# Optimization experiments

Measured on AMD Instinct MI355X. Metric: run time of the kernel, lower is better.

Reference implementation:

```python
import jax, jax.numpy as jnp
import numpy as np

EPS = 1e-12  # matches torch F.normalize default eps

def _l2_normalize(x):
    # torch.nn.functional.normalize: x / max(||x||_2, eps)
    n = jnp.sqrt(jnp.sum(x * x, axis=-1, keepdims=True))
    return x / jnp.maximum(n, EPS)

def setup_inputs() -> dict:
    key = jax.random.key(0)
    kq, kk, kv = jax.random.split(key, 3)
    B, N, M, C = 8, 4096, 4096, 256
    return {
        "query": jax.random.normal(kq, (B, N, C), dtype=jnp.float32),
        "key": jax.random.normal(kk, (B, M, C), dtype=jnp.float32),
        "value": jax.random.normal(kv, (B, M, C), dtype=jnp.float32),
    }

def reference(query, key, value):
    B, N, C = query.shape
    q = _l2_normalize(query)          # (B, N, C)
    k = _l2_normalize(key)            # (B, M, C)
    kv = jnp.einsum('bmc,bmd->bcd', k, value)   # (B, C, C)
    context = jnp.einsum('bnc,bcd->bnd', q, kv) # (B, N, C)
    return context / N
```

## Files before the change

### kernel.cpp

```cpp
#include <hip/hip_runtime.h>

typedef __attribute__((ext_vector_type(4))) float v4f;
typedef __attribute__((ext_vector_type(8))) short short8;
typedef unsigned short u16;
typedef __attribute__((ext_vector_type(4))) unsigned short u16x4;
typedef __attribute__((ext_vector_type(8))) unsigned short u16x8;

#define CDIM 256
#define NB 8
#define NN 4096
#define MM 4096

static __device__ __forceinline__ u16 f2bf(float f) {
  unsigned u = __float_as_uint(f);
  u = (u + 0x7fffu + ((u >> 16) & 1u)) >> 16;
  return (u16)u;
}
static __device__ __forceinline__ float bf2f(u16 h) {
  return __uint_as_float(((unsigned)h) << 16);
}

__global__ __launch_bounds__(256) void knorm_kernel(const float* __restrict__ key,
                                                    float* __restrict__ sk) {
  int t = threadIdx.x;
  int lane = t & 63;
  int r = blockIdx.x * 4 + (t >> 6);
  const v4f x = *(const v4f*)(key + (size_t)r * CDIM + lane * 4);
  float ss = x[0]*x[0] + x[1]*x[1] + x[2]*x[2] + x[3]*x[3];
  #pragma unroll
  for (int m = 1; m < 64; m <<= 1) ss += __shfl_xor(ss, m);
  if (lane == 0) sk[r] = 1.0f / fmaxf(sqrtf(ss), 1e-12f);
}

__global__ __launch_bounds__(512, 2) void kv_kernel(const float* __restrict__ key,
                                                    const float* __restrict__ value,
                                                    const float* __restrict__ sk,
                                                    u16* __restrict__ partial, int KC) {
  __shared__ __align__(16) u16 knT[256 * 64];
  __shared__ __align__(16) u16 vT[256 * 64];
  int t = threadIdx.x;
  int b = blockIdx.y, s = blockIdx.x;
  int w = t >> 6, lane = t & 63, lo = lane & 15, hi = lane >> 4;
  int cstage = t & 255, wq = t >> 8;

  v4f acc[2][16];
  #pragma unroll
  for (int i = 0; i < 2; i++)
    #pragma unroll
    for (int d = 0; d < 16; d++) acc[i][d] = (v4f){0.f, 0.f, 0.f, 0.f};

  int nsc = KC >> 6;
  for (int sc = 0; sc < nsc; ++sc) {
    int mbase = s * KC + sc * 64;
    #pragma unroll
    for (int it = 0; it < 8; ++it) {
      int ml0 = it * 8 + wq * 4;
      int gr = b * MM + mbase + ml0;
      size_t grow = (size_t)gr * CDIM + cstage;
      float k0 = key[grow], k1 = key[grow + CDIM], k2 = key[grow + 2 * CDIM], k3 = key[grow + 3 * CDIM];
      float s0 = sk[gr], s1 = sk[gr + 1], s2 = sk[gr + 2], s3 = sk[gr + 3];
      u16x4 kn = { f2bf(k0 * s0), f2bf(k1 * s1), f2bf(k2 * s2), f2bf(k3 * s3) };
      int idx = (cstage * 64 + ml0) ^ ((cstage & 7) << 3);
      *(u16x4*)&knT[idx] = kn;
      float v0 = value[grow], v1 = value[grow + CDIM], v2 = value[grow + 2 * CDIM], v3 = value[grow + 3 * CDIM];
      u16x4 vn = { f2bf(v0), f2bf(v1), f2bf(v2), f2bf(v3) };
      *(u16x4*)&vT[idx] = vn;
    }
    __syncthreads();
    #pragma unroll
    for (int kk = 0; kk < 64; kk += 32) {
      int acol = kk + hi * 8;
      int r0 = w * 32 + lo, r1 = w * 32 + 16 + lo;
      short8 a0 = *(const short8*)&knT[(r0 * 64 + acol) ^ ((r0 & 7) << 3)];
      short8 a1 = *(const short8*)&knT[(r1 * 64 + acol) ^ ((r1 & 7) << 3)];
      #pragma unroll
      for (int dt = 0; dt < 16; ++dt) {
        int drow = dt * 16 + lo;
        short8 bb = *(const short8*)&vT[(drow * 64 + acol) ^ ((drow & 7) << 3)];
        acc[0][dt] = __builtin_amdgcn_mfma_f32_16x16x32_bf16(bb, a0, acc[0][dt], 0, 0, 0);
        acc[1][dt] = __builtin_amdgcn_mfma_f32_16x16x32_bf16(bb, a1, acc[1][dt], 0, 0, 0);
      }
    }
    __syncthreads();
  }
  size_t base = ((size_t)(s * NB + b)) << 16;
  #pragma unroll
  for (int i = 0; i < 2; i++) {
    int cc = w * 32 + i * 16 + lo;
    #pragma unroll
    for (int dt = 0; dt < 16; ++dt) {
      int dd = dt * 16 + hi * 4;
      #pragma unroll
      for (int r = 0; r < 4; r++)
        partial[base + (size_t)(dd + r) * 256 + cc] = f2bf(acc[i][dt][r]);
    }
  }
}

__global__ __launch_bounds__(256) void red_kernel(const u16* __restrict__ partial,
                                                  u16* __restrict__ kvT, int splits) {
  int j = blockIdx.x * 256 + threadIdx.x;
  int b = j >> 13;
  int e0 = (j & 8191) * 8;
  size_t off = ((size_t)b << 16) + e0;
  const float inv = 1.0f / 4096.0f;
  float sum[8] = {0.f, 0.f, 0.f, 0.f, 0.f, 0.f, 0.f, 0.f};
  for (int s = 0; s < splits; ++s) {
    u16x8 p = *(const u16x8*)&partial[(((size_t)s * NB) << 16) + off];
    #pragma unroll
    for (int x = 0; x < 8; ++x) sum[x] += bf2f(p[x]);
  }
  u16x8 o;
  #pragma unroll
  for (int x = 0; x < 8; ++x) o[x] = f2bf(sum[x] * inv);
  *(u16x8*)&kvT[off] = o;
}

__global__ __launch_bounds__(512) void ctx_kernel(const float* __restrict__ query,
                                                  const u16* __restrict__ kvT,
                                                  float* __restrict__ out) {
  __shared__ __align__(16) u16 qn[2][16 * 256];
  int t = threadIdx.x;
  int b = blockIdx.y;
  int tile0 = blockIdx.x * 4;
  int w = t >> 6, lane = t & 63, lo = lane & 15, hi = lane >> 4;
  int row = t >> 5, l32 = t & 31;
  const float* qbase = query + (size_t)b * NN * CDIM + (size_t)row * CDIM + l32 * 8;

  const float* qr0 = qbase + (size_t)(tile0 * 16) * CDIM;
  v4f x0 = *(const v4f*)qr0;
  v4f x1 = *(const v4f*)(qr0 + 4);

  const u16* kvb = kvT + ((size_t)b << 16);
  short8 Bf[2][8];
  #pragma unroll
  for (int i = 0; i < 2; i++) {
    int dr = (2 * w + i) * 16 + lo;
    #pragma unroll
    for (int kc = 0; kc < 8; kc++)
      Bf[i][kc] = *(const short8*)&kvb[(size_t)dr * 256 + kc * 32 + 8 * hi];
  }

  {
    float ss = x0[0]*x0[0] + x0[1]*x0[1] + x0[2]*x0[2] + x0[3]*x0[3]
             + x1[0]*x1[0] + x1[1]*x1[1] + x1[2]*x1[2] + x1[3]*x1[3];
    #pragma unroll
    for (int m = 1; m < 32; m <<= 1) ss += __shfl_xor(ss, m);
    float sc = 1.0f / fmaxf(sqrtf(ss), 1e-12f);
    u16x8 qb;
    qb[0] = f2bf(x0[0] * sc); qb[1] = f2bf(x0[1] * sc);
    qb[2] = f2bf(x0[2] * sc); qb[3] = f2bf(x0[3] * sc);
    qb[4] = f2bf(x1[0] * sc); qb[5] = f2bf(x1[1] * sc);
    qb[6] = f2bf(x1[2] * sc); qb[7] = f2bf(x1[3] * sc);
    *(u16x8*)&qn[0][(row * 256 + l32 * 8) ^ ((row & 7) << 3)] = qb;
  }

  int cur = 0;
  #pragma unroll
  for (int nt = 0; nt < 4; ++nt) {
    v4f p0, p1;
    if (nt < 3) {
      const float* qr = qbase + (size_t)((tile0 + nt + 1) * 16) * CDIM;
      p0 = *(const v4f*)qr;
      p1 = *(const v4f*)(qr + 4);
    }
    __syncthreads();
    short8 Af[8];
    #pragma unroll
    for (int kc = 0; kc < 8; kc++)
      Af[kc] = *(const short8*)&qn[cur][(lo * 256 + kc * 32 + 8 * hi) ^ ((lo & 7) << 3)];
    v4f acc0 = (v4f){0.f, 0.f, 0.f, 0.f};
    v4f acc1 = (v4f){0.f, 0.f, 0.f, 0.f};
    #pragma unroll
    for (int kc = 0; kc < 8; kc++) {
      acc0 = __builtin_amdgcn_mfma_f32_16x16x32_bf16(Af[kc], Bf[0][kc], acc0, 0, 0, 0);
      acc1 = __builtin_amdgcn_mfma_f32_16x16x32_bf16(Af[kc], Bf[1][kc], acc1, 0, 0, 0);
    }
    int n0 = (tile0 + nt) * 16;
    #pragma unroll
    for (int r = 0; r < 4; r++) {
      size_t ro = (size_t)(b * NN + n0 + 4 * hi + r) * CDIM;
      out[ro + (2 * w) * 16 + lo] = acc0[r];
      out[ro + (2 * w + 1) * 16 + lo] = acc1[r];
    }
    if (nt < 3) {
      float ss = p0[0]*p0[0] + p0[1]*p0[1] + p0[2]*p0[2] + p0[3]*p0[3]
               + p1[0]*p1[0] + p1[1]*p1[1] + p1[2]*p1[2] + p1[3]*p1[3];
      #pragma unroll
      for (int m = 1; m < 32; m <<= 1) ss += __shfl_xor(ss, m);
      float sc = 1.0f / fmaxf(sqrtf(ss), 1e-12f);
      u16x8 qb;
      qb[0] = f2bf(p0[0] * sc); qb[1] = f2bf(p0[1] * sc);
      qb[2] = f2bf(p0[2] * sc); qb[3] = f2bf(p0[3] * sc);
      qb[4] = f2bf(p1[0] * sc); qb[5] = f2bf(p1[1] * sc);
      qb[6] = f2bf(p1[2] * sc); qb[7] = f2bf(p1[3] * sc);
      *(u16x8*)&qn[cur ^ 1][(row * 256 + l32 * 8) ^ ((row & 7) << 3)] = qb;
      cur ^= 1;
    }
  }
}

extern "C" void kernel_launch(void* const* d_in, const int* in_sizes, int n_in,
                              void* d_out, int out_size, void* d_ws, size_t ws_size,
                              hipStream_t stream) {
  const float* q = (const float*)d_in[0];
  const float* k = (const float*)d_in[1];
  const float* v = (const float*)d_in[2];
  float* out = (float*)d_out;

  int splits = 32;
  while (splits > 2) {
    size_t need = 131072ull + ((size_t)splits + 1ull) * 1048576ull;
    if (need <= ws_size) break;
    splits >>= 1;
  }
  float* s_k = (float*)d_ws;
  u16* partial = (u16*)((char*)d_ws + 131072);
  u16* kvT = (u16*)((char*)d_ws + 131072 + (size_t)splits * 1048576ull);

  knorm_kernel<<<dim3(8192), dim3(256), 0, stream>>>(k, s_k);
  kv_kernel<<<dim3(splits, NB), dim3(512), 0, stream>>>(k, v, s_k, partial, MM / splits);
  red_kernel<<<dim3(256), dim3(256), 0, stream>>>(partial, kvT, splits);
  ctx_kernel<<<dim3(64, NB), dim3(512), 0, stream>>>(q, kvT, out);
}
```

Measured before the change: 64.00 us.

## Fuse key norm into kv kernel, double-buffer LDS, vectorize loads with shuffle transpose

```diff
diff --git a/kernel.cpp b/kernel.cpp
--- a/kernel.cpp
+++ b/kernel.cpp
@@ -3,6 +3,8 @@
 typedef __attribute__((ext_vector_type(4))) float v4f;
 typedef __attribute__((ext_vector_type(8))) short short8;
 typedef unsigned short u16;
+typedef unsigned int u32;
+typedef __attribute__((ext_vector_type(2))) unsigned int u32x2;
 typedef __attribute__((ext_vector_type(4))) unsigned short u16x4;
 typedef __attribute__((ext_vector_type(8))) unsigned short u16x8;
 
@@ -19,29 +21,39 @@
 static __device__ __forceinline__ float bf2f(u16 h) {
   return __uint_as_float(((unsigned)h) << 16);
 }
-
-__global__ __launch_bounds__(256) void knorm_kernel(const float* __restrict__ key,
-                                                    float* __restrict__ sk) {
-  int t = threadIdx.x;
-  int lane = t & 63;
-  int r = blockIdx.x * 4 + (t >> 6);
-  const v4f x = *(const v4f*)(key + (size_t)r * CDIM + lane * 4);
-  float ss = x[0]*x[0] + x[1]*x[1] + x[2]*x[2] + x[3]*x[3];
-  #pragma unroll
-  for (int m = 1; m < 64; m <<= 1) ss += __shfl_xor(ss, m);
-  if (lane == 0) sk[r] = 1.0f / fmaxf(sqrtf(ss), 1e-12f);
-}
-
-__global__ __launch_bounds__(512, 2) void kv_kernel(const float* __restrict__ key,
-                                                    const float* __restrict__ value,
-                                                    const float* __restrict__ sk,
-                                                    u16* __restrict__ partial, int KC) {
-  __shared__ __align__(16) u16 knT[256 * 64];
-  __shared__ __align__(16) u16 vT[256 * 64];
+static __device__ __forceinline__ u32 pack2(float a, float b) {
+  return (u32)f2bf(a) | ((u32)f2bf(b) << 16);
+}
+
+static __device__ __forceinline__ u32x2 xpose4(u32 A, u32 B, int hi) {
+  u32 tA = (u32)__shfl_xor((int)A, 32);
+  u32 tB = (u32)__shfl_xor((int)B, 32);
+  u32 U = (hi < 2) ? A : tB;
+  u32 V = (hi < 2) ? tA : B;
+  u32 tU = (u32)__shfl_xor((int)U, 16);
+  u32 tV = (u32)__shfl_xor((int)V, 16);
+  u32 Up, Vp;
+  if ((hi & 1) == 0) {
+    Up = (U & 0xffffu) | (tU << 16);
+    Vp = (V & 0xffffu) | (tV << 16);
+  } else {
+    Up = (tU >> 16) | (U & 0xffff0000u);
+    Vp = (tV >> 16) | (V & 0xffff0000u);
+  }
+  return (u32x2){Up, Vp};
+}
+
+__global__ __launch_bounds__(512) void kv_kernel(const float* __restrict__ key,
+                                                 const float* __restrict__ value,
+                                                 u16* __restrict__ partial, int KC) {
+  __shared__ __align__(16) u16 knT[2][256 * 64];
+  __shared__ __align__(16) u16 vT[2][256 * 64];
   int t = threadIdx.x;
   int b = blockIdx.y, s = blockIdx.x;
   int w = t >> 6, lane = t & 63, lo = lane & 15, hi = lane >> 4;
-  int cstage = t & 255, wq = t >> 8;
+
+  const float* kbase = key + ((size_t)b * MM + (size_t)s * KC) * CDIM;
+  const float* vbase = value + ((size_t)b * MM + (size_t)s * KC) * CDIM;
 
   v4f acc[2][16];
   #pragma unroll
@@ -49,40 +61,72 @@
     #pragma unroll
     for (int d = 0; d < 16; d++) acc[i][d] = (v4f){0.f, 0.f, 0.f, 0.f};
 
-  int nsc = KC >> 6;
-  for (int sc = 0; sc < nsc; ++sc) {
-    int mbase = s * KC + sc * 64;
-    #pragma unroll
-    for (int it = 0; it < 8; ++it) {
-      int ml0 = it * 8 + wq * 4;
-      int gr = b * MM + mbase + ml0;
-      size_t grow = (size_t)gr * CDIM + cstage;
-      float k0 = key[grow], k1 = key[grow + CDIM], k2 = key[grow + 2 * CDIM], k3 = key[grow + 3 * CDIM];
-      float s0 = sk[gr], s1 = sk[gr + 1], s2 = sk[gr + 2], s3 = sk[gr + 3];
-      u16x4 kn = { f2bf(k0 * s0), f2bf(k1 * s1), f2bf(k2 * s2), f2bf(k3 * s3) };
-      int idx = (cstage * 64 + ml0) ^ ((cstage & 7) << 3);
-      *(u16x4*)&knT[idx] = kn;
-      float v0 = value[grow], v1 = value[grow + CDIM], v2 = value[grow + 2 * CDIM], v3 = value[grow + 3 * CDIM];
-      u16x4 vn = { f2bf(v0), f2bf(v1), f2bf(v2), f2bf(v3) };
-      *(u16x4*)&vT[idx] = vn;
-    }
-    __syncthreads();
+  v4f kq[4], vq[4];
+
+  auto LOADS = [&](int sc, int it) {
+    int row = sc * 64 + w * 8 + it * 4 + hi;
+    const float* kr = kbase + (size_t)row * CDIM + lo * 4;
+    const float* vr = vbase + (size_t)row * CDIM + lo * 4;
+    #pragma unroll
+    for (int qt = 0; qt < 4; ++qt) {
+      kq[qt] = *(const v4f*)(kr + qt * 64);
+      vq[qt] = *(const v4f*)(vr + qt * 64);
+    }
+  };
+  auto STORE = [&](int bufi, int it) {
+    int m0 = w * 8 + it * 4;
+    float ss = 0.f;
+    #pragma unroll
+    for (int qt = 0; qt < 4; ++qt)
+      ss += kq[qt][0]*kq[qt][0] + kq[qt][1]*kq[qt][1] + kq[qt][2]*kq[qt][2] + kq[qt][3]*kq[qt][3];
+    #pragma unroll
+    for (int m = 1; m < 16; m <<= 1) ss += __shfl_xor(ss, m);
+    float sc_ = 1.0f / fmaxf(sqrtf(ss), 1e-12f);
+    #pragma unroll
+    for (int qt = 0; qt < 4; ++qt) {
+      int c = qt * 64 + lo * 4 + hi;
+      int idx = (c * 64 + m0) ^ ((c & 7) << 3);
+      u32x2 ko = xpose4(pack2(kq[qt][0] * sc_, kq[qt][1] * sc_),
+                        pack2(kq[qt][2] * sc_, kq[qt][3] * sc_), hi);
+      *(u32x2*)&knT[bufi][idx] = ko;
+      u32x2 vo = xpose4(pack2(vq[qt][0], vq[qt][1]),
+                        pack2(vq[qt][2], vq[qt][3]), hi);
+      *(u32x2*)&vT[bufi][idx] = vo;
+    }
+  };
+  auto MF = [&](const u16* KB, const u16* VB) {
     #pragma unroll
     for (int kk = 0; kk < 64; kk += 32) {
       int acol = kk + hi * 8;
       int r0 = w * 32 + lo, r1 = w * 32 + 16 + lo;
-      short8 a0 = *(const short8*)&knT[(r0 * 64 + acol) ^ ((r0 & 7) << 3)];
-      short8 a1 = *(const short8*)&knT[(r1 * 64 + acol) ^ ((r1 & 7) << 3)];
+      short8 a0 = *(const short8*)&KB[(r0 * 64 + acol) ^ ((r0 & 7) << 3)];
+      short8 a1 = *(const short8*)&KB[(r1 * 64 + acol) ^ ((r1 & 7) << 3)];
       #pragma unroll
       for (int dt = 0; dt < 16; ++dt) {
         int drow = dt * 16 + lo;
-        short8 bb = *(const short8*)&vT[(drow * 64 + acol) ^ ((drow & 7) << 3)];
+        short8 bb = *(const short8*)&VB[(drow * 64 + acol) ^ ((drow & 7) << 3)];
         acc[0][dt] = __builtin_amdgcn_mfma_f32_16x16x32_bf16(bb, a0, acc[0][dt], 0, 0, 0);
         acc[1][dt] = __builtin_amdgcn_mfma_f32_16x16x32_bf16(bb, a1, acc[1][dt], 0, 0, 0);
       }
     }
+  };
+
+  int nsc = KC >> 6;
+  LOADS(0, 0); STORE(0, 0);
+  LOADS(0, 1); STORE(0, 1);
+  __syncthreads();
+  for (int sc = 0; sc < nsc; ++sc) {
+    int nb = (sc + 1) & 1;
+    if (sc + 1 < nsc) LOADS(sc + 1, 0);
+    MF(knT[sc & 1], vT[sc & 1]);
+    if (sc + 1 < nsc) {
+      STORE(nb, 0);
+      LOADS(sc + 1, 1);
+      STORE(nb, 1);
+    }
     __syncthreads();
   }
+
   size_t base = ((size_t)(s * NB + b)) << 16;
   #pragma unroll
   for (int i = 0; i < 2; i++) {
@@ -210,16 +254,14 @@
 
   int splits = 32;
   while (splits > 2) {
-    size_t need = 131072ull + ((size_t)splits + 1ull) * 1048576ull;
+    size_t need = ((size_t)splits + 1ull) * 1048576ull;
     if (need <= ws_size) break;
     splits >>= 1;
   }
-  float* s_k = (float*)d_ws;
-  u16* partial = (u16*)((char*)d_ws + 131072);
-  u16* kvT = (u16*)((char*)d_ws + 131072 + (size_t)splits * 1048576ull);
-
-  knorm_kernel<<<dim3(8192), dim3(256), 0, stream>>>(k, s_k);
-  kv_kernel<<<dim3(splits, NB), dim3(512), 0, stream>>>(k, v, s_k, partial, MM / splits);
+  u16* partial = (u16*)d_ws;
+  u16* kvT = (u16*)((char*)d_ws + (size_t)splits * 1048576ull);
+
+  kv_kernel<<<dim3(splits, NB), dim3(512), 0, stream>>>(k, v, partial, MM / splits);
   red_kernel<<<dim3(256), dim3(256), 0, stream>>>(partial, kvT, splits);
   ctx_kernel<<<dim3(64, NB), dim3(512), 0, stream>>>(q, kvT, out);
 }
```

New measurement: 56.83 us. 11.2% less time.
